# Optimization experiments

Measured on AMD Instinct MI355X. Metric: run time of the kernel, lower is better.

Reference implementation:

```python
import jax, jax.numpy as jnp
import numpy as np

B, SEG, MEM, D, E, H = 4, 1024, 1024, 128, 128, 8  # model_dim == embed_dim required by module
TOTAL = SEG + MEM


def sinusoid_pos(length, e):
    # Transformer-XL relative sinusoid table, then flipped so row 0 = largest distance
    p = jnp.arange(length, dtype=jnp.float32)[:, None]
    j = jnp.arange(e, dtype=jnp.float32)[None, :]
    ang = p / jnp.power(jnp.float32(10000.0), 2.0 * j / e)
    enc = jnp.where((jnp.arange(e) % 2 == 0)[None, :], jnp.sin(ang), jnp.cos(ang))
    return enc[::-1]


def circulant_shift(b, shift):
    # b: (B, H, S, W). Row i of the index matrix is the rolled arange shifted by (shift - i).
    W = b.shape[-1]
    S = b.shape[-2]
    idx = jnp.roll(jnp.arange(W), shift)[::-1]
    idx2 = jnp.concatenate([idx, idx])
    win = idx2[jnp.arange(S)[:, None] + jnp.arange(W)[None, :]][:, ::-1]  # (S, W)
    return jnp.take_along_axis(b, win[None, None, :, :], axis=3)


def setup_inputs() -> dict:
    key = jax.random.key(0)
    ks = jax.random.split(key, 11)
    w = 0.02  # small init for linear weights (Linear default-ish scale)
    return {
        "x": jax.random.normal(ks[0], (B, SEG, D), dtype=jnp.float32),
        "mem": jax.random.normal(ks[1], (B, MEM, D), dtype=jnp.float32),
        "att_mask": jnp.zeros((SEG, TOTAL), dtype=bool),  # unused by the module's forward
        "u1": jax.random.normal(ks[2], (H, 1, E), dtype=jnp.float32),
        "u2": jax.random.normal(ks[3], (H, 1, E), dtype=jnp.float32),
        "w_q": jax.random.normal(ks[4], (D, H * E), dtype=jnp.float32) * w,
        "w_kv": jax.random.normal(ks[5], (D, 2 * H * E), dtype=jnp.float32) * w,
        "w_r": jax.random.normal(ks[6], (D, H * E), dtype=jnp.float32) * w,
        "w_mlp": jax.random.normal(ks[7], (H * E, D), dtype=jnp.float32) * w,
        "ln_g": jnp.ones((D,), dtype=jnp.float32),
        "ln_b": jnp.zeros((D,), dtype=jnp.float32),
    }


def reference(x, mem, att_mask, u1, u2, w_q, w_kv, w_r, w_mlp, ln_g, ln_b):
    bsz, seg, d = x.shape
    h = jnp.concatenate((mem, x), axis=1)          # (B, total, D)
    total = h.shape[1]
    mem_len = total - seg

    # NB: the original uses .view without transpose -> plain row-major reshape
    q = (x @ w_q).reshape(bsz, -1, seg, d)          # (B, H, S, E)
    kv = (h @ w_kv).reshape(2 * bsz, -1, total, d)  # (2B, H, T, E)
    k, v = kv[:bsz], kv[bsz:]

    pos = sinusoid_pos(total, d)                    # buffer pos[-total:]
    r = (pos @ w_r).reshape(-1, total, d)           # (H, T, E)

    b = jnp.einsum('bhse,hte->bhst', q, r)
    b = circulant_shift(b, -seg + 1)

    qk = jnp.einsum('bhse,bhte->bhst', q, k)
    u1k = jnp.einsum('he,bhte->bht', u1[:, 0], k)[:, :, None, :]
    u2r = jnp.einsum('he,hte->ht', u2[:, 0], r)[None, :, None, :]

    score = qk + b + u1k + u2r                      # (B, H, S, T)
    tri = (jnp.arange(total)[None, :] - jnp.arange(seg)[:, None]) <= mem_len
    score = jnp.where(tri[None, None], score, 0.0) / jnp.sqrt(jnp.float32(d))
    score = jnp.where(score == 0.0, -jnp.inf, score)  # faithful zeros->-inf trick
    score = jax.nn.softmax(score, axis=-1)

    att = jnp.einsum('bhst,bhte->bhse', score, v).reshape(bsz, seg, -1)
    y = att @ w_mlp + x
    mu = jnp.mean(y, axis=-1, keepdims=True)
    var = jnp.mean((y - mu) ** 2, axis=-1, keepdims=True)
    return (y - mu) / jnp.sqrt(var + 1e-5) * ln_g + ln_b
```

## Files before the change

### kernel.cpp

```cpp
#include <hip/hip_runtime.h>
#include <hip/hip_bf16.h>
#include <stdint.h>

typedef __bf16 bf16;
typedef __attribute__((ext_vector_type(8))) __bf16 bf16x8;
typedef __attribute__((ext_vector_type(4))) float f32x4;

#define KSC 0.12764932952880681f

__device__ __forceinline__ f32x4 MFMA(bf16x8 a, bf16x8 b, f32x4 c) {
  return __builtin_amdgcn_mfma_f32_16x16x32_bf16(a, b, c, 0, 0, 0);
}

__device__ __forceinline__ void GLL16(const void* g, void* l) {
  __builtin_amdgcn_global_load_lds(
      (const __attribute__((address_space(1))) void*)g,
      (__attribute__((address_space(3))) void*)l, 16, 0, 0);
}

__device__ __forceinline__ bf16 tobf(float f) { return (bf16)f; }

__global__ __launch_bounds__(256) void k_prep(
    const float* __restrict__ x, const float* __restrict__ mm,
    const float* __restrict__ wq, const float* __restrict__ wkv,
    const float* __restrict__ wr, const float* __restrict__ wmlp,
    bf16* __restrict__ posb, bf16* __restrict__ wq_bt, bf16* __restrict__ wkv_bt,
    bf16* __restrict__ wr_bt, bf16* __restrict__ wmlp_bt,
    bf16* __restrict__ xb, bf16* __restrict__ memb)
{
  int id = blockIdx.x * 256 + threadIdx.x;
  if (id < 262144) {
    int t = id >> 7, j = id & 127;
    float p = (float)(2047 - t);
    float ang = p * exp2f(-(float)j * 0.20762050593046264f);
    float v = ((j & 1) == 0) ? sinf(ang) : cosf(ang);
    posb[id] = tobf(v);
    return;
  }
  id -= 262144;
  if (id < 131072) { int n = id >> 7, k = id & 127; wq_bt[id] = tobf(wq[k * 1024 + n]); return; }
  id -= 131072;
  if (id < 262144) { int n = id >> 7, k = id & 127; wkv_bt[id] = tobf(wkv[k * 2048 + n]); return; }
  id -= 262144;
  if (id < 131072) { int n = id >> 7, k = id & 127; wr_bt[id] = tobf(wr[k * 1024 + n]); return; }
  id -= 131072;
  if (id < 131072) { int n = id >> 10, k = id & 1023; wmlp_bt[id] = tobf(wmlp[k * 128 + n]); return; }
  id -= 131072;
  if (id < 524288) { xb[id] = tobf(x[id]); return; }
  id -= 524288;
  if (id < 524288) { memb[id] = tobf(mm[id]); return; }
}

template <int MODE>
__global__ __launch_bounds__(256, 2) void k_proj(
    const bf16* __restrict__ asrc, const bf16* __restrict__ asrc2,
    const bf16* __restrict__ wbt, bf16* __restrict__ out0, bf16* __restrict__ out1,
    float oscale)
{
  __shared__ bf16 As[64 * 128];
  __shared__ bf16 Bs[128 * 128];
  const int m0 = blockIdx.x * 64;
  const int n0 = blockIdx.y * 128;
  const int tid = threadIdx.x;
  const int w = tid >> 6, lane = tid & 63, g = lane >> 4, c = lane & 15;

#pragma unroll
  for (int it = 0; it < 4; ++it) {
    int ch = w * 256 + it * 64 + lane;
    int row = ch >> 4, cc = ch & 15;
    int scc = cc ^ (row & 7);
    const bf16* src;
    if (MODE == 1) {
      int rg = m0 + row;
      int bb = rg >> 11, t = rg & 2047;
      src = (t < 1024) ? (asrc2 + (size_t)(bb * 1024 + t) * 128)
                       : (asrc + (size_t)(bb * 1024 + (t - 1024)) * 128);
    } else {
      src = asrc + (size_t)(m0 + row) * 128;
    }
    GLL16(src + scc * 8, (char*)As + (w * 256 + it * 64) * 16);
  }
#pragma unroll
  for (int it = 0; it < 8; ++it) {
    int ch = w * 512 + it * 64 + lane;
    int n = ch >> 4, cc = ch & 15;
    int scc = cc ^ (n & 7);
    GLL16(wbt + (size_t)(n0 + n) * 128 + scc * 8, (char*)Bs + (w * 512 + it * 64) * 16);
  }
  __syncthreads();

  f32x4 acc[8] = {};
#pragma unroll
  for (int kk = 0; kk < 4; ++kk) {
    bf16x8 a = *(const bf16x8*)((const char*)As + (16 * w + c) * 256 + (((4 * kk + g) ^ (c & 7)) << 4));
#pragma unroll
    for (int fo = 0; fo < 8; ++fo) {
      bf16x8 b = *(const bf16x8*)((const char*)Bs + (16 * fo + c) * 256 + (((4 * kk + g) ^ (c & 7)) << 4));
      acc[fo] = MFMA(a, b, acc[fo]);
    }
  }

#pragma unroll
  for (int fo = 0; fo < 8; ++fo) {
#pragma unroll
    for (int j = 0; j < 4; ++j) {
      int rg = m0 + 16 * w + 4 * g + j;
      int cg = n0 + 16 * fo + c;
      bf16 v = tobf(acc[fo][j] * oscale);
      if (MODE == 0) {
        int b = rg >> 10, s2 = rg & 1023;
        int nn = s2 >> 7;
        int s = ((s2 & 127) << 3) | (cg >> 7);
        int e = cg & 127;
        out0[((size_t)((b * 8 + nn) * 1024 + s)) * 128 + e] = v;
      } else if (MODE == 1) {
        int bb = rg >> 11, t = rg & 2047;
        int nn = (t >> 7) & 7;
        int hlf = (t >> 10) & 1;
        int t2 = ((t & 127) << 4) | (cg >> 7);
        int e = cg & 127;
        if (bb < 2)
          out0[((size_t)(((2 * bb + hlf) * 8 + nn) * 2048 + t2)) * 128 + e] = v;
        else
          out1[((size_t)(((2 * (bb - 2) + hlf) * 8 + nn) * 2048 + t2)) * 128 + e] = v;
      } else {
        int nn = rg >> 8;
        int t = ((rg & 255) << 3) | (cg >> 7);
        int e = cg & 127;
        out0[((size_t)(nn * 2048 + t)) * 128 + e] = v;
      }
    }
  }
}

__global__ __launch_bounds__(256) void k_vtrans(const bf16* __restrict__ vh, bf16* __restrict__ vht)
{
  __shared__ bf16 T[64][72];
  int bt = blockIdx.x * 64, be = blockIdx.y * 64, bh = blockIdx.z;
  const bf16* src = vh + (size_t)bh * 2048 * 128;
  bf16* dst = vht + (size_t)bh * 128 * 2048;
#pragma unroll
  for (int i2 = 0; i2 < 2; ++i2) {
    int ch = i2 * 256 + threadIdx.x;
    int tt = ch >> 3, cc = ch & 7;
    bf16x8 v = *(const bf16x8*)(src + (size_t)(bt + tt) * 128 + be + cc * 8);
    *(bf16x8*)&T[tt][cc * 8] = v;
  }
  __syncthreads();
#pragma unroll
  for (int i2 = 0; i2 < 2; ++i2) {
    int ch = i2 * 256 + threadIdx.x;
    int ee = ch >> 3, c2 = ch & 7;
    bf16x8 o;
#pragma unroll
    for (int m = 0; m < 8; ++m) o[m] = T[c2 * 8 + m][ee];
    *(bf16x8*)(dst + (size_t)(be + ee) * 2048 + bt + c2 * 8) = o;
  }
}

__global__ __launch_bounds__(256) void k_uterms(
    const bf16* __restrict__ kh, const bf16* __restrict__ rh,
    const float* __restrict__ u1, const float* __restrict__ u2,
    float* __restrict__ uu)
{
  int id = blockIdx.x * 256 + threadIdx.x;
  int n = (id >> 11) & 7;
  int t = id & 2047;
  const bf16* kp = kh + (size_t)id * 128;
  const bf16* rp = rh + ((size_t)(n * 2048 + t)) * 128;
  const float* u1p = u1 + n * 128;
  const float* u2p = u2 + n * 128;
  float s = 0.f;
#pragma unroll
  for (int c0 = 0; c0 < 128; c0 += 8) {
    bf16x8 kv = *(const bf16x8*)(kp + c0);
    bf16x8 rv = *(const bf16x8*)(rp + c0);
#pragma unroll
    for (int j = 0; j < 8; ++j) s += (float)kv[j] * u1p[c0 + j] + (float)rv[j] * u2p[c0 + j];
  }
  uu[id] = s * KSC;
}

__global__ __launch_bounds__(256, 2) void k_flash(
    const bf16* __restrict__ qh, const bf16* __restrict__ kh,
    const bf16* __restrict__ vht, const bf16* __restrict__ rh,
    const float* __restrict__ uu, bf16* __restrict__ att2)
{
  __shared__ bf16 Ks[2][64 * 128];
  __shared__ bf16 Vs[2][64 * 128];
  __shared__ bf16 QRS[4][16 * 90];

  const int x = blockIdx.x;
  const int bh = x & 31;
  const int qb = (x < 256) ? (x >> 5) : (15 - ((x - 256) >> 5));
  const int ib = bh >> 3, nh = bh & 7;
  const int s0 = qb * 64;
  const int tid = threadIdx.x;
  const int w = tid >> 6, lane = tid & 63, g = lane >> 4, c = lane & 15;

  const bf16* qbase = qh + (size_t)bh * 1024 * 128;
  const bf16* kbase = kh + (size_t)bh * 2048 * 128;
  const bf16* vbase = vht + (size_t)bh * 128 * 2048;
  const bf16* rbase = rh + (size_t)nh * 2048 * 128;
  const float* uup  = uu + bh * 2048;

  const int nt = qb + 17;

  auto stage = [&](int tile) {
    int pb = tile & 1;
    int t0s = tile * 64;
    char* Kd = (char*)Ks[pb];
    char* Vd = (char*)Vs[pb];
#pragma unroll
    for (int it = 0; it < 4; ++it) {
      int ch = w * 256 + it * 64 + lane;
      int row = ch >> 4, cc2 = ch & 15;
      GLL16(kbase + (size_t)(t0s + row) * 128 + ((cc2 ^ (row & 7)) * 8), Kd + ch * 16);
    }
#pragma unroll
    for (int it = 0; it < 4; ++it) {
      int ch = w * 256 + it * 64 + lane;
      int e = ch >> 3, tc = ch & 7;
      GLL16(vbase + (size_t)e * 2048 + t0s + ((tc ^ (e & 7)) * 8), Vd + ch * 16);
    }
  };

  bf16x8 qf[4];
  {
    int srow = s0 + 16 * w + c;
#pragma unroll
    for (int kk = 0; kk < 4; ++kk)
      qf[kk] = *(const bf16x8*)(qbase + (size_t)srow * 128 + kk * 32 + g * 8);
  }

  f32x4 Ot[8] = {};
  float m_j[4], l_j[4];
#pragma unroll
  for (int j = 0; j < 4; ++j) { m_j[j] = -1e30f; l_j[j] = 0.f; }

  stage(0);

  for (int tt = 0; tt < nt; ++tt) {
    const int t0 = tt * 64;
    const int pb = tt & 1;
    __syncthreads();
    if (tt + 1 < nt) stage(tt + 1);

    bf16x8 rf[5][4];
    const int wb = t0 - s0 - 16 * w - 1040 + 4096;
#pragma unroll
    for (int f2 = 0; f2 < 5; ++f2) {
      int u = (wb + 16 * f2 + c) & 2047;
      const bf16* rrow = rbase + (size_t)u * 128;
#pragma unroll
      for (int kk = 0; kk < 4; ++kk) rf[f2][kk] = *(const bf16x8*)(rrow + kk * 32 + g * 8);
    }

    const bf16* Kc = Ks[pb];
    const bf16* Vc = Vs[pb];

    f32x4 sacc[4] = {};
    __builtin_amdgcn_s_setprio(1);
#pragma unroll
    for (int kk = 0; kk < 4; ++kk) {
#pragma unroll
      for (int f = 0; f < 4; ++f) {
        bf16x8 kf = *(const bf16x8*)((const char*)Kc + (16 * f + c) * 256 + (((4 * kk + g) ^ (c & 7)) << 4));
        sacc[f] = MFMA(qf[kk], kf, sacc[f]);
      }
    }
    f32x4 bacc[5] = {};
#pragma unroll
    for (int f2 = 0; f2 < 5; ++f2)
#pragma unroll
      for (int kk = 0; kk < 4; ++kk)
        bacc[f2] = MFMA(qf[kk], rf[f2][kk], bacc[f2]);
    __builtin_amdgcn_s_setprio(0);

    bf16* qrw = QRS[w];
#pragma unroll
    for (int f2 = 0; f2 < 5; ++f2)
#pragma unroll
      for (int j = 0; j < 4; ++j)
        qrw[(4 * g + j) * 90 + 16 * f2 + c] = tobf(bacc[f2][j]);

    float uuv[4];
#pragma unroll
    for (int f = 0; f < 4; ++f) uuv[f] = uup[t0 + 16 * f + c];

    const bool lastT = (tt == nt - 1);
    float zv[4][4];
#pragma unroll
    for (int f = 0; f < 4; ++f) {
#pragma unroll
      for (int j = 0; j < 4; ++j) {
        int il = 4 * g + j;
        float bias = (float)qrw[il * 90 + (16 * f + c - il + 15)];
        float z = sacc[f][j] + bias + uuv[f];
        if (lastT && (16 * f + c > 16 * w + il)) z = -1e30f;
        zv[f][j] = z;
      }
    }
    float alpha[4];
#pragma unroll
    for (int j = 0; j < 4; ++j) {
      float tm = fmaxf(fmaxf(zv[0][j], zv[1][j]), fmaxf(zv[2][j], zv[3][j]));
#pragma unroll
      for (int d = 1; d < 16; d <<= 1) tm = fmaxf(tm, __shfl_xor(tm, d));
      float mn = fmaxf(m_j[j], tm);
      alpha[j] = exp2f(m_j[j] - mn);
      m_j[j] = mn;
      float ps = 0.f;
#pragma unroll
      for (int f = 0; f < 4; ++f) { float pp = exp2f(zv[f][j] - mn); zv[f][j] = pp; ps += pp; }
#pragma unroll
      for (int d = 1; d < 16; d <<= 1) ps += __shfl_xor(ps, d);
      l_j[j] = l_j[j] * alpha[j] + ps;
    }
#pragma unroll
    for (int fo = 0; fo < 8; ++fo)
#pragma unroll
      for (int j = 0; j < 4; ++j) Ot[fo][j] *= alpha[j];

    bf16* pw = qrw;
#pragma unroll
    for (int f = 0; f < 4; ++f)
#pragma unroll
      for (int j = 0; j < 4; ++j) {
        int il = 4 * g + j;
        pw[il * 64 + ((((2 * f + (c >> 3)) ^ (il & 7)) << 3) | (c & 7))] = tobf(zv[f][j]);
      }

    __builtin_amdgcn_s_setprio(1);
#pragma unroll
    for (int kk2 = 0; kk2 < 2; ++kk2) {
      bf16x8 pa = *(const bf16x8*)(pw + c * 64 + (((4 * kk2 + g) ^ (c & 7)) << 3));
#pragma unroll
      for (int fo = 0; fo < 8; ++fo) {
        int e = 16 * fo + c;
        bf16x8 vf = *(const bf16x8*)((const char*)Vc + e * 128 + (((4 * kk2 + g) ^ (c & 7)) << 4));
        Ot[fo] = MFMA(pa, vf, Ot[fo]);
      }
    }
    __builtin_amdgcn_s_setprio(0);
  }

  bf16* ob = att2 + (size_t)ib * 1024 * 1024;
#pragma unroll
  for (int j = 0; j < 4; ++j) {
    int sg = s0 + 16 * w + 4 * g + j;
    size_t rowb = (size_t)(nh * 128 + (sg >> 3)) * 1024 + ((sg & 7) << 7);
    float inv = 1.f / l_j[j];
#pragma unroll
    for (int fo = 0; fo < 8; ++fo)
      ob[rowb + 16 * fo + c] = tobf(Ot[fo][j] * inv);
  }
}

__global__ __launch_bounds__(256, 2) void k_mlp(
    const bf16* __restrict__ att2, const bf16* __restrict__ wmlp_bt,
    const float* __restrict__ x, const float* __restrict__ lng, const float* __restrict__ lnb,
    float* __restrict__ out)
{
  __shared__ bf16 As[64 * 128];
  __shared__ bf16 Bs[128 * 128];
  const int m0 = blockIdx.x * 64;
  const int tid = threadIdx.x;
  const int w = tid >> 6, lane = tid & 63, g = lane >> 4, c = lane & 15;

  f32x4 acc[8] = {};
  for (int ks = 0; ks < 8; ++ks) {
    int k0 = ks * 128;
    __syncthreads();
#pragma unroll
    for (int it = 0; it < 4; ++it) {
      int ch = w * 256 + it * 64 + lane;
      int row = ch >> 4, cc = ch & 15;
      GLL16(att2 + (size_t)(m0 + row) * 1024 + k0 + ((cc ^ (row & 7)) * 8),
            (char*)As + (w * 256 + it * 64) * 16);
    }
#pragma unroll
    for (int it = 0; it < 8; ++it) {
      int ch = w * 512 + it * 64 + lane;
      int n = ch >> 4, cc = ch & 15;
      GLL16(wmlp_bt + (size_t)n * 1024 + k0 + ((cc ^ (n & 7)) * 8),
            (char*)Bs + (w * 512 + it * 64) * 16);
    }
    __syncthreads();
#pragma unroll
    for (int kk = 0; kk < 4; ++kk) {
      bf16x8 a = *(const bf16x8*)((const char*)As + (16 * w + c) * 256 + (((4 * kk + g) ^ (c & 7)) << 4));
#pragma unroll
      for (int fo = 0; fo < 8; ++fo) {
        bf16x8 b = *(const bf16x8*)((const char*)Bs + (16 * fo + c) * 256 + (((4 * kk + g) ^ (c & 7)) << 4));
        acc[fo] = MFMA(a, b, acc[fo]);
      }
    }
  }
#pragma unroll
  for (int j = 0; j < 4; ++j) {
    int rg = m0 + 16 * w + 4 * g + j;
    float y[8];
    float s1 = 0.f, s2 = 0.f;
#pragma unroll
    for (int fo = 0; fo < 8; ++fo) {
      float v = acc[fo][j] + x[(size_t)rg * 128 + 16 * fo + c];
      y[fo] = v; s1 += v; s2 += v * v;
    }
#pragma unroll
    for (int d = 1; d < 16; d <<= 1) { s1 += __shfl_xor(s1, d); s2 += __shfl_xor(s2, d); }
    float mu = s1 * 0.0078125f;
    float var = s2 * 0.0078125f - mu * mu;
    float rs = rsqrtf(var + 1e-5f);
#pragma unroll
    for (int fo = 0; fo < 8; ++fo) {
      int e = 16 * fo + c;
      out[(size_t)rg * 128 + e] = (y[fo] - mu) * rs * lng[e] + lnb[e];
    }
  }
}

extern "C" void kernel_launch(void* const* d_in, const int* in_sizes, int n_in,
                              void* d_out, int out_size, void* d_ws, size_t ws_size,
                              hipStream_t stream)
{
  const float* x    = (const float*)d_in[0];
  const float* mm   = (const float*)d_in[1];
  const float* u1   = (const float*)d_in[3];
  const float* u2   = (const float*)d_in[4];
  const float* wq   = (const float*)d_in[5];
  const float* wkv  = (const float*)d_in[6];
  const float* wr   = (const float*)d_in[7];
  const float* wmlp = (const float*)d_in[8];
  const float* lng  = (const float*)d_in[9];
  const float* lnb  = (const float*)d_in[10];
  float* out = (float*)d_out;

  char* p = (char*)d_ws;
  bf16* posb    = (bf16*)p;  p += (size_t)262144 * 2;
  bf16* wq_bt   = (bf16*)p;  p += (size_t)131072 * 2;
  bf16* wkv_bt  = (bf16*)p;  p += (size_t)262144 * 2;
  bf16* wr_bt   = (bf16*)p;  p += (size_t)131072 * 2;
  bf16* wmlp_bt = (bf16*)p;  p += (size_t)131072 * 2;
  bf16* xb      = (bf16*)p;  p += (size_t)524288 * 2;
  bf16* memb    = (bf16*)p;  p += (size_t)524288 * 2;
  bf16* qh      = (bf16*)p;  p += (size_t)4 * 8 * 1024 * 128 * 2;
  bf16* kh      = (bf16*)p;  p += (size_t)4 * 8 * 2048 * 128 * 2;
  bf16* vh      = (bf16*)p;  p += (size_t)4 * 8 * 2048 * 128 * 2;
  bf16* vht     = (bf16*)p;  p += (size_t)4 * 8 * 2048 * 128 * 2;
  bf16* rh      = (bf16*)p;  p += (size_t)8 * 2048 * 128 * 2;
  float* uu     = (float*)p; p += (size_t)65536 * 4;
  bf16* att2    = (bf16*)p;  p += (size_t)4 * 1024 * 1024 * 2;

  k_prep<<<dim3(7680), dim3(256), 0, stream>>>(x, mm, wq, wkv, wr, wmlp,
                                               posb, wq_bt, wkv_bt, wr_bt, wmlp_bt, xb, memb);
  k_proj<0><<<dim3(64, 8),   dim3(256), 0, stream>>>(xb,  (const bf16*)nullptr, wq_bt,  qh, (bf16*)nullptr, KSC);
  k_proj<1><<<dim3(128, 16), dim3(256), 0, stream>>>(xb,  memb,                 wkv_bt, kh, vh,             1.0f);
  k_proj<2><<<dim3(32, 8),   dim3(256), 0, stream>>>(posb,(const bf16*)nullptr, wr_bt,  rh, (bf16*)nullptr, 1.0f);
  k_vtrans<<<dim3(32, 2, 32), dim3(256), 0, stream>>>(vh, vht);
  k_uterms<<<dim3(256), dim3(256), 0, stream>>>(kh, rh, u1, u2, uu);
  k_flash<<<dim3(512), dim3(256), 0, stream>>>(qh, kh, vht, rh, uu, att2);
  k_mlp<<<dim3(64), dim3(256), 0, stream>>>(att2, wmlp_bt, x, lng, lnb, out);
}
```

Baseline: 318.4 us.

## Prefetch R tiles across iterations, merge aux kernels, vectorize prep conversions

In the flash kernel, the next iteration's relative-position R fragments and u-terms are now prefetched during the current iteration, and the last R fragment is reused from the previous window, so global loads stop sitting on the critical path. The softmax reductions are restructured so all four rows' shuffles are interleaved, which raises instruction-level parallelism. The V transpose and u-term kernels are fused into one launch. The prep kernel now reads weights coalesced and converts x/mem with vector loads. The prefetch raises register pressure in the flash kernel, which could reduce occupancy.

```diff
diff --git a/kernel.cpp b/kernel.cpp
--- a/kernel.cpp
+++ b/kernel.cpp
@@ -4,6 +4,7 @@
 
 typedef __bf16 bf16;
 typedef __attribute__((ext_vector_type(8))) __bf16 bf16x8;
+typedef __attribute__((ext_vector_type(4))) __bf16 bf16x4;
 typedef __attribute__((ext_vector_type(4))) float f32x4;
 
 #define KSC 0.12764932952880681f
@@ -38,17 +39,26 @@
     return;
   }
   id -= 262144;
-  if (id < 131072) { int n = id >> 7, k = id & 127; wq_bt[id] = tobf(wq[k * 1024 + n]); return; }
+  if (id < 131072) { int k = id >> 10, n = id & 1023; wq_bt[n * 128 + k] = tobf(wq[id]); return; }
   id -= 131072;
-  if (id < 262144) { int n = id >> 7, k = id & 127; wkv_bt[id] = tobf(wkv[k * 2048 + n]); return; }
+  if (id < 262144) { int k = id >> 11, n = id & 2047; wkv_bt[n * 128 + k] = tobf(wkv[id]); return; }
   id -= 262144;
-  if (id < 131072) { int n = id >> 7, k = id & 127; wr_bt[id] = tobf(wr[k * 1024 + n]); return; }
+  if (id < 131072) { int k = id >> 10, n = id & 1023; wr_bt[n * 128 + k] = tobf(wr[id]); return; }
   id -= 131072;
-  if (id < 131072) { int n = id >> 10, k = id & 1023; wmlp_bt[id] = tobf(wmlp[k * 128 + n]); return; }
+  if (id < 131072) { int k = id >> 7, n = id & 127; wmlp_bt[n * 1024 + k] = tobf(wmlp[id]); return; }
   id -= 131072;
-  if (id < 524288) { xb[id] = tobf(x[id]); return; }
-  id -= 524288;
-  if (id < 524288) { memb[id] = tobf(mm[id]); return; }
+  if (id < 131072) {
+    f32x4 v = *(const f32x4*)(x + (size_t)id * 4);
+    bf16x4 o; o[0]=tobf(v[0]); o[1]=tobf(v[1]); o[2]=tobf(v[2]); o[3]=tobf(v[3]);
+    *(bf16x4*)(xb + (size_t)id * 4) = o;
+    return;
+  }
+  id -= 131072;
+  if (id < 131072) {
+    f32x4 v = *(const f32x4*)(mm + (size_t)id * 4);
+    bf16x4 o; o[0]=tobf(v[0]); o[1]=tobf(v[1]); o[2]=tobf(v[2]); o[3]=tobf(v[3]);
+    *(bf16x4*)(memb + (size_t)id * 4) = o;
+  }
 }
 
 template <int MODE>
@@ -133,52 +143,53 @@
   }
 }
 
-__global__ __launch_bounds__(256) void k_vtrans(const bf16* __restrict__ vh, bf16* __restrict__ vht)
-{
-  __shared__ bf16 T[64][72];
-  int bt = blockIdx.x * 64, be = blockIdx.y * 64, bh = blockIdx.z;
-  const bf16* src = vh + (size_t)bh * 2048 * 128;
-  bf16* dst = vht + (size_t)bh * 128 * 2048;
-#pragma unroll
-  for (int i2 = 0; i2 < 2; ++i2) {
-    int ch = i2 * 256 + threadIdx.x;
-    int tt = ch >> 3, cc = ch & 7;
-    bf16x8 v = *(const bf16x8*)(src + (size_t)(bt + tt) * 128 + be + cc * 8);
-    *(bf16x8*)&T[tt][cc * 8] = v;
-  }
-  __syncthreads();
-#pragma unroll
-  for (int i2 = 0; i2 < 2; ++i2) {
-    int ch = i2 * 256 + threadIdx.x;
-    int ee = ch >> 3, c2 = ch & 7;
-    bf16x8 o;
-#pragma unroll
-    for (int m = 0; m < 8; ++m) o[m] = T[c2 * 8 + m][ee];
-    *(bf16x8*)(dst + (size_t)(be + ee) * 2048 + bt + c2 * 8) = o;
-  }
-}
-
-__global__ __launch_bounds__(256) void k_uterms(
+__global__ __launch_bounds__(256) void k_aux(
+    const bf16* __restrict__ vh, bf16* __restrict__ vht,
     const bf16* __restrict__ kh, const bf16* __restrict__ rh,
     const float* __restrict__ u1, const float* __restrict__ u2,
     float* __restrict__ uu)
 {
-  int id = blockIdx.x * 256 + threadIdx.x;
-  int n = (id >> 11) & 7;
-  int t = id & 2047;
-  const bf16* kp = kh + (size_t)id * 128;
-  const bf16* rp = rh + ((size_t)(n * 2048 + t)) * 128;
-  const float* u1p = u1 + n * 128;
-  const float* u2p = u2 + n * 128;
-  float s = 0.f;
-#pragma unroll
-  for (int c0 = 0; c0 < 128; c0 += 8) {
-    bf16x8 kv = *(const bf16x8*)(kp + c0);
-    bf16x8 rv = *(const bf16x8*)(rp + c0);
-#pragma unroll
-    for (int j = 0; j < 8; ++j) s += (float)kv[j] * u1p[c0 + j] + (float)rv[j] * u2p[c0 + j];
-  }
-  uu[id] = s * KSC;
+  __shared__ bf16 T[64][72];
+  const int bid = blockIdx.x;
+  if (bid < 2048) {
+    int bt = (bid & 31) * 64, be = ((bid >> 5) & 1) * 64, bh = bid >> 6;
+    const bf16* src = vh + (size_t)bh * 2048 * 128;
+    bf16* dst = vht + (size_t)bh * 128 * 2048;
+#pragma unroll
+    for (int i2 = 0; i2 < 2; ++i2) {
+      int ch = i2 * 256 + threadIdx.x;
+      int tt = ch >> 3, cc = ch & 7;
+      bf16x8 v = *(const bf16x8*)(src + (size_t)(bt + tt) * 128 + be + cc * 8);
+      *(bf16x8*)&T[tt][cc * 8] = v;
+    }
+    __syncthreads();
+#pragma unroll
+    for (int i2 = 0; i2 < 2; ++i2) {
+      int ch = i2 * 256 + threadIdx.x;
+      int ee = ch >> 3, c2 = ch & 7;
+      bf16x8 o;
+#pragma unroll
+      for (int m = 0; m < 8; ++m) o[m] = T[c2 * 8 + m][ee];
+      *(bf16x8*)(dst + (size_t)(be + ee) * 2048 + bt + c2 * 8) = o;
+    }
+  } else {
+    int id = (bid - 2048) * 256 + threadIdx.x;
+    int n = (id >> 11) & 7;
+    int t = id & 2047;
+    const bf16* kp = kh + (size_t)id * 128;
+    const bf16* rp = rh + ((size_t)(n * 2048 + t)) * 128;
+    const float* u1p = u1 + n * 128;
+    const float* u2p = u2 + n * 128;
+    float s = 0.f;
+#pragma unroll
+    for (int c0 = 0; c0 < 128; c0 += 8) {
+      bf16x8 kv = *(const bf16x8*)(kp + c0);
+      bf16x8 rv = *(const bf16x8*)(rp + c0);
+#pragma unroll
+      for (int j = 0; j < 8; ++j) s += (float)kv[j] * u1p[c0 + j] + (float)rv[j] * u2p[c0 + j];
+    }
+    uu[id] = s * KSC;
+  }
 }
 
 __global__ __launch_bounds__(256, 2) void k_flash(
@@ -233,6 +244,21 @@
       qf[kk] = *(const bf16x8*)(qbase + (size_t)srow * 128 + kk * 32 + g * 8);
   }
 
+  bf16x8 rf[5][4];
+  float uuv[4], uun[4];
+  {
+    const int wb0 = -s0 - 16 * w - 1040 + 4096;
+#pragma unroll
+    for (int f2 = 0; f2 < 5; ++f2) {
+      int u = (wb0 + 16 * f2 + c) & 2047;
+      const bf16* rrow = rbase + (size_t)u * 128;
+#pragma unroll
+      for (int kk = 0; kk < 4; ++kk) rf[f2][kk] = *(const bf16x8*)(rrow + kk * 32 + g * 8);
+    }
+#pragma unroll
+    for (int f = 0; f < 4; ++f) uuv[f] = uup[16 * f + c];
+  }
+
   f32x4 Ot[8] = {};
   float m_j[4], l_j[4];
 #pragma unroll
@@ -241,20 +267,10 @@
   stage(0);
 
   for (int tt = 0; tt < nt; ++tt) {
-    const int t0 = tt * 64;
     const int pb = tt & 1;
+    const bool notlast = (tt + 1 < nt);
     __syncthreads();
-    if (tt + 1 < nt) stage(tt + 1);
-
-    bf16x8 rf[5][4];
-    const int wb = t0 - s0 - 16 * w - 1040 + 4096;
-#pragma unroll
-    for (int f2 = 0; f2 < 5; ++f2) {
-      int u = (wb + 16 * f2 + c) & 2047;
-      const bf16* rrow = rbase + (size_t)u * 128;
-#pragma unroll
-      for (int kk = 0; kk < 4; ++kk) rf[f2][kk] = *(const bf16x8*)(rrow + kk * 32 + g * 8);
-    }
+    if (notlast) stage(tt + 1);
 
     const bf16* Kc = Ks[pb];
     const bf16* Vc = Vs[pb];
@@ -284,11 +300,22 @@
       for (int j = 0; j < 4; ++j)
         qrw[(4 * g + j) * 90 + 16 * f2 + c] = tobf(bacc[f2][j]);
 
-    float uuv[4];
-#pragma unroll
-    for (int f = 0; f < 4; ++f) uuv[f] = uup[t0 + 16 * f + c];
-
-    const bool lastT = (tt == nt - 1);
+    if (notlast) {
+#pragma unroll
+      for (int kk = 0; kk < 4; ++kk) rf[0][kk] = rf[4][kk];
+      const int wbn = 64 * (tt + 1) - s0 - 16 * w - 1040 + 4096;
+#pragma unroll
+      for (int f2 = 1; f2 < 5; ++f2) {
+        int u = (wbn + 16 * f2 + c) & 2047;
+        const bf16* rrow = rbase + (size_t)u * 128;
+#pragma unroll
+        for (int kk = 0; kk < 4; ++kk) rf[f2][kk] = *(const bf16x8*)(rrow + kk * 32 + g * 8);
+      }
+#pragma unroll
+      for (int f = 0; f < 4; ++f) uun[f] = uup[64 * (tt + 1) + 16 * f + c];
+    }
+
+    const bool lastT = !notlast;
     float zv[4][4];
 #pragma unroll
     for (int f = 0; f < 4; ++f) {
@@ -301,22 +328,32 @@
         zv[f][j] = z;
       }
     }
-    float alpha[4];
+    float tm[4], ps[4], alpha[4];
+#pragma unroll
+    for (int j = 0; j < 4; ++j)
+      tm[j] = fmaxf(fmaxf(zv[0][j], zv[1][j]), fmaxf(zv[2][j], zv[3][j]));
+#pragma unroll
+    for (int d = 1; d < 16; d <<= 1)
+#pragma unroll
+      for (int j = 0; j < 4; ++j) tm[j] = fmaxf(tm[j], __shfl_xor(tm[j], d));
 #pragma unroll
     for (int j = 0; j < 4; ++j) {
-      float tm = fmaxf(fmaxf(zv[0][j], zv[1][j]), fmaxf(zv[2][j], zv[3][j]));
-#pragma unroll
-      for (int d = 1; d < 16; d <<= 1) tm = fmaxf(tm, __shfl_xor(tm, d));
-      float mn = fmaxf(m_j[j], tm);
+      float mn = fmaxf(m_j[j], tm[j]);
       alpha[j] = exp2f(m_j[j] - mn);
       m_j[j] = mn;
-      float ps = 0.f;
-#pragma unroll
-      for (int f = 0; f < 4; ++f) { float pp = exp2f(zv[f][j] - mn); zv[f][j] = pp; ps += pp; }
-#pragma unroll
-      for (int d = 1; d < 16; d <<= 1) ps += __shfl_xor(ps, d);
-      l_j[j] = l_j[j] * alpha[j] + ps;
-    }
+    }
+#pragma unroll
+    for (int j = 0; j < 4; ++j) {
+      ps[j] = 0.f;
+#pragma unroll
+      for (int f = 0; f < 4; ++f) { float pp = exp2f(zv[f][j] - m_j[j]); zv[f][j] = pp; ps[j] += pp; }
+    }
+#pragma unroll
+    for (int d = 1; d < 16; d <<= 1)
+#pragma unroll
+      for (int j = 0; j < 4; ++j) ps[j] += __shfl_xor(ps[j], d);
+#pragma unroll
+    for (int j = 0; j < 4; ++j) l_j[j] = l_j[j] * alpha[j] + ps[j];
 #pragma unroll
     for (int fo = 0; fo < 8; ++fo)
 #pragma unroll
@@ -343,6 +380,9 @@
       }
     }
     __builtin_amdgcn_s_setprio(0);
+
+#pragma unroll
+    for (int f = 0; f < 4; ++f) uuv[f] = uun[f];
   }
 
   bf16* ob = att2 + (size_t)ib * 1024 * 1024;
@@ -452,13 +492,12 @@
   float* uu     = (float*)p; p += (size_t)65536 * 4;
   bf16* att2    = (bf16*)p;  p += (size_t)4 * 1024 * 1024 * 2;
 
-  k_prep<<<dim3(7680), dim3(256), 0, stream>>>(x, mm, wq, wkv, wr, wmlp,
+  k_prep<<<dim3(4608), dim3(256), 0, stream>>>(x, mm, wq, wkv, wr, wmlp,
                                                posb, wq_bt, wkv_bt, wr_bt, wmlp_bt, xb, memb);
   k_proj<0><<<dim3(64, 8),   dim3(256), 0, stream>>>(xb,  (const bf16*)nullptr, wq_bt,  qh, (bf16*)nullptr, KSC);
   k_proj<1><<<dim3(128, 16), dim3(256), 0, stream>>>(xb,  memb,                 wkv_bt, kh, vh,             1.0f);
   k_proj<2><<<dim3(32, 8),   dim3(256), 0, stream>>>(posb,(const bf16*)nullptr, wr_bt,  rh, (bf16*)nullptr, 1.0f);
-  k_vtrans<<<dim3(32, 2, 32), dim3(256), 0, stream>>>(vh, vht);
-  k_uterms<<<dim3(256), dim3(256), 0, stream>>>(kh, rh, u1, u2, uu);
+  k_aux<<<dim3(2304), dim3(256), 0, stream>>>(vh, vht, kh, rh, u1, u2, uu);
   k_flash<<<dim3(512), dim3(256), 0, stream>>>(qh, kh, vht, rh, uu, att2);
   k_mlp<<<dim3(64), dim3(256), 0, stream>>>(att2, wmlp_bt, x, lng, lnb, out);
 }
```

Result: faster. 308.8 us (-3.0%).

## Fold u-bias terms into shifted queries, drop uterms kernel, rework flash softmax

Applied to the files above, without the earlier changes.

The u1/u2 bias terms are folded algebraically into two pre-scaled query copies (q+u1 for the K product, q+u2 for the R product), which removes the separate k_uterms kernel and the per-tile uu loads. The R table is padded with 64 wrapped rows so the flash kernel can walk it with precomputed pointers and prefetch the next tile's R fragments, replacing the per-tile modulo addressing. MFMA operands are swapped so each lane owns one query row, the softmax uses a single running max with a lazy rescale that is skipped while the max grows by less than a threshold, and K/V staging uses precomputed incremental pointers. The prep kernel now uses coalesced reads for the weight transposes and vectorised x/mem conversion. These changes add a second query buffer and raise register pressure from prefetched R fragments.

```diff
diff --git a/kernel.cpp b/kernel.cpp
--- a/kernel.cpp
+++ b/kernel.cpp
@@ -4,6 +4,7 @@
 
 typedef __bf16 bf16;
 typedef __attribute__((ext_vector_type(8))) __bf16 bf16x8;
+typedef __attribute__((ext_vector_type(4))) __bf16 bf16x4;
 typedef __attribute__((ext_vector_type(4))) float f32x4;
 
 #define KSC 0.12764932952880681f
@@ -38,24 +39,33 @@
     return;
   }
   id -= 262144;
-  if (id < 131072) { int n = id >> 7, k = id & 127; wq_bt[id] = tobf(wq[k * 1024 + n]); return; }
+  if (id < 131072) { int k = id >> 10, n = id & 1023; wq_bt[n * 128 + k] = tobf(wq[id]); return; }
   id -= 131072;
-  if (id < 262144) { int n = id >> 7, k = id & 127; wkv_bt[id] = tobf(wkv[k * 2048 + n]); return; }
+  if (id < 262144) { int k = id >> 11, n = id & 2047; wkv_bt[n * 128 + k] = tobf(wkv[id]); return; }
   id -= 262144;
-  if (id < 131072) { int n = id >> 7, k = id & 127; wr_bt[id] = tobf(wr[k * 1024 + n]); return; }
+  if (id < 131072) { int k = id >> 10, n = id & 1023; wr_bt[n * 128 + k] = tobf(wr[id]); return; }
   id -= 131072;
-  if (id < 131072) { int n = id >> 10, k = id & 1023; wmlp_bt[id] = tobf(wmlp[k * 128 + n]); return; }
+  if (id < 131072) { int k = id >> 7, n = id & 127; wmlp_bt[n * 1024 + k] = tobf(wmlp[id]); return; }
   id -= 131072;
-  if (id < 524288) { xb[id] = tobf(x[id]); return; }
-  id -= 524288;
-  if (id < 524288) { memb[id] = tobf(mm[id]); return; }
+  if (id < 131072) {
+    f32x4 v = *(const f32x4*)(x + (size_t)id * 4);
+    bf16x4 o; o[0]=tobf(v[0]); o[1]=tobf(v[1]); o[2]=tobf(v[2]); o[3]=tobf(v[3]);
+    *(bf16x4*)(xb + (size_t)id * 4) = o;
+    return;
+  }
+  id -= 131072;
+  if (id < 131072) {
+    f32x4 v = *(const f32x4*)(mm + (size_t)id * 4);
+    bf16x4 o; o[0]=tobf(v[0]); o[1]=tobf(v[1]); o[2]=tobf(v[2]); o[3]=tobf(v[3]);
+    *(bf16x4*)(memb + (size_t)id * 4) = o;
+  }
 }
 
 template <int MODE>
 __global__ __launch_bounds__(256, 2) void k_proj(
     const bf16* __restrict__ asrc, const bf16* __restrict__ asrc2,
     const bf16* __restrict__ wbt, bf16* __restrict__ out0, bf16* __restrict__ out1,
-    float oscale)
+    const float* __restrict__ u1, const float* __restrict__ u2)
 {
   __shared__ bf16 As[64 * 128];
   __shared__ bf16 Bs[128 * 128];
@@ -106,19 +116,22 @@
     for (int j = 0; j < 4; ++j) {
       int rg = m0 + 16 * w + 4 * g + j;
       int cg = n0 + 16 * fo + c;
-      bf16 v = tobf(acc[fo][j] * oscale);
+      float av = acc[fo][j];
       if (MODE == 0) {
         int b = rg >> 10, s2 = rg & 1023;
         int nn = s2 >> 7;
         int s = ((s2 & 127) << 3) | (cg >> 7);
         int e = cg & 127;
-        out0[((size_t)((b * 8 + nn) * 1024 + s)) * 128 + e] = v;
+        size_t idx = ((size_t)((b * 8 + nn) * 1024 + s)) * 128 + e;
+        out0[idx] = tobf((av + u1[nn * 128 + e]) * KSC);
+        out1[idx] = tobf((av + u2[nn * 128 + e]) * KSC);
       } else if (MODE == 1) {
         int bb = rg >> 11, t = rg & 2047;
         int nn = (t >> 7) & 7;
         int hlf = (t >> 10) & 1;
         int t2 = ((t & 127) << 4) | (cg >> 7);
         int e = cg & 127;
+        bf16 v = tobf(av);
         if (bb < 2)
           out0[((size_t)(((2 * bb + hlf) * 8 + nn) * 2048 + t2)) * 128 + e] = v;
         else
@@ -127,7 +140,9 @@
         int nn = rg >> 8;
         int t = ((rg & 255) << 3) | (cg >> 7);
         int e = cg & 127;
-        out0[((size_t)(nn * 2048 + t)) * 128 + e] = v;
+        bf16 v = tobf(av);
+        out0[((size_t)(nn * 2112 + t)) * 128 + e] = v;
+        if (t < 64) out0[((size_t)(nn * 2112 + 2048 + t)) * 128 + e] = v;
       }
     }
   }
@@ -158,37 +173,14 @@
   }
 }
 
-__global__ __launch_bounds__(256) void k_uterms(
-    const bf16* __restrict__ kh, const bf16* __restrict__ rh,
-    const float* __restrict__ u1, const float* __restrict__ u2,
-    float* __restrict__ uu)
-{
-  int id = blockIdx.x * 256 + threadIdx.x;
-  int n = (id >> 11) & 7;
-  int t = id & 2047;
-  const bf16* kp = kh + (size_t)id * 128;
-  const bf16* rp = rh + ((size_t)(n * 2048 + t)) * 128;
-  const float* u1p = u1 + n * 128;
-  const float* u2p = u2 + n * 128;
-  float s = 0.f;
-#pragma unroll
-  for (int c0 = 0; c0 < 128; c0 += 8) {
-    bf16x8 kv = *(const bf16x8*)(kp + c0);
-    bf16x8 rv = *(const bf16x8*)(rp + c0);
-#pragma unroll
-    for (int j = 0; j < 8; ++j) s += (float)kv[j] * u1p[c0 + j] + (float)rv[j] * u2p[c0 + j];
-  }
-  uu[id] = s * KSC;
-}
-
 __global__ __launch_bounds__(256, 2) void k_flash(
-    const bf16* __restrict__ qh, const bf16* __restrict__ kh,
-    const bf16* __restrict__ vht, const bf16* __restrict__ rh,
-    const float* __restrict__ uu, bf16* __restrict__ att2)
+    const bf16* __restrict__ qhk, const bf16* __restrict__ qhr,
+    const bf16* __restrict__ kh, const bf16* __restrict__ vht,
+    const bf16* __restrict__ rhe, bf16* __restrict__ att2)
 {
   __shared__ bf16 Ks[2][64 * 128];
   __shared__ bf16 Vs[2][64 * 128];
-  __shared__ bf16 QRS[4][16 * 90];
+  __shared__ char QRS[4][2688];
 
   const int x = blockIdx.x;
   const int bh = x & 31;
@@ -198,66 +190,80 @@
   const int tid = threadIdx.x;
   const int w = tid >> 6, lane = tid & 63, g = lane >> 4, c = lane & 15;
 
-  const bf16* qbase = qh + (size_t)bh * 1024 * 128;
+  const bf16* qkb  = qhk + (size_t)bh * 1024 * 128;
+  const bf16* qrb  = qhr + (size_t)bh * 1024 * 128;
   const bf16* kbase = kh + (size_t)bh * 2048 * 128;
   const bf16* vbase = vht + (size_t)bh * 128 * 2048;
-  const bf16* rbase = rh + (size_t)nh * 2048 * 128;
-  const float* uup  = uu + bh * 2048;
+  const bf16* rbase = rhe + (size_t)nh * 2112 * 128;
 
   const int nt = qb + 17;
 
-  auto stage = [&](int tile) {
-    int pb = tile & 1;
-    int t0s = tile * 64;
-    char* Kd = (char*)Ks[pb];
-    char* Vd = (char*)Vs[pb];
-#pragma unroll
-    for (int it = 0; it < 4; ++it) {
-      int ch = w * 256 + it * 64 + lane;
-      int row = ch >> 4, cc2 = ch & 15;
-      GLL16(kbase + (size_t)(t0s + row) * 128 + ((cc2 ^ (row & 7)) * 8), Kd + ch * 16);
-    }
-#pragma unroll
-    for (int it = 0; it < 4; ++it) {
-      int ch = w * 256 + it * 64 + lane;
-      int e = ch >> 3, tc = ch & 7;
-      GLL16(vbase + (size_t)e * 2048 + t0s + ((tc ^ (e & 7)) * 8), Vd + ch * 16);
-    }
+  const bf16 *kp0, *kp1, *vp0, *vp1, *vp2, *vp3;
+  {
+    int ch0 = w * 256 + lane;
+    int ch1 = ch0 + 64;
+    int r0 = ch0 >> 4, cc0 = ch0 & 15;
+    int r1 = ch1 >> 4, cc1 = ch1 & 15;
+    kp0 = kbase + (size_t)r0 * 128 + (cc0 ^ (r0 & 7)) * 8;
+    kp1 = kbase + (size_t)r1 * 128 + (cc1 ^ (r1 & 7)) * 8;
+    int e0 = ch0 >> 3, t0c = ch0 & 7;
+    int e1 = ch1 >> 3, t1c = ch1 & 7;
+    int e2 = e0 + 16, e3 = e1 + 16;
+    vp0 = vbase + (size_t)e0 * 2048 + (t0c ^ (e0 & 7)) * 8;
+    vp1 = vbase + (size_t)e1 * 2048 + (t1c ^ (e1 & 7)) * 8;
+    vp2 = vbase + (size_t)e2 * 2048 + (t0c ^ (e2 & 7)) * 8;
+    vp3 = vbase + (size_t)e3 * 2048 + (t1c ^ (e3 & 7)) * 8;
+  }
+  const int dof = (w * 256 + lane) * 16;
+
+  auto stage = [&](char* Kd, char* Vd) {
+    GLL16(kp0, Kd + dof);
+    GLL16(kp1, Kd + dof + 1024);
+    GLL16(kp0 + 1024, Kd + dof + 2048);
+    GLL16(kp1 + 1024, Kd + dof + 3072);
+    GLL16(vp0, Vd + dof);
+    GLL16(vp1, Vd + dof + 1024);
+    GLL16(vp2, Vd + dof + 2048);
+    GLL16(vp3, Vd + dof + 3072);
+    kp0 += 8192; kp1 += 8192;
+    vp0 += 64; vp1 += 64; vp2 += 64; vp3 += 64;
   };
 
-  bf16x8 qf[4];
+  bf16x8 qfK[4], qfR[4];
   {
     int srow = s0 + 16 * w + c;
 #pragma unroll
-    for (int kk = 0; kk < 4; ++kk)
-      qf[kk] = *(const bf16x8*)(qbase + (size_t)srow * 128 + kk * 32 + g * 8);
+    for (int kk = 0; kk < 4; ++kk) {
+      qfK[kk] = *(const bf16x8*)(qkb + (size_t)srow * 128 + kk * 32 + g * 8);
+      qfR[kk] = *(const bf16x8*)(qrb + (size_t)srow * 128 + kk * 32 + g * 8);
+    }
+  }
+
+  bf16x8 rf[5][4];
+  const bf16* rp[5];
+  {
+    const int L0 = 1008 - s0 - 16 * w + c;
+#pragma unroll
+    for (int f2 = 0; f2 < 5; ++f2) {
+      rp[f2] = rbase + (size_t)(L0 + 16 * f2) * 128 + g * 8;
+#pragma unroll
+      for (int kk = 0; kk < 4; ++kk) rf[f2][kk] = *(const bf16x8*)(rp[f2] + kk * 32);
+      rp[f2] += 64 * 128;
+    }
   }
 
   f32x4 Ot[8] = {};
-  float m_j[4], l_j[4];
-#pragma unroll
-  for (int j = 0; j < 4; ++j) { m_j[j] = -1e30f; l_j[j] = 0.f; }
-
-  stage(0);
+  float m_r = -1e30f, l_r = 0.f;
+
+  stage((char*)Ks[0], (char*)Vs[0]);
 
   for (int tt = 0; tt < nt; ++tt) {
-    const int t0 = tt * 64;
-    const int pb = tt & 1;
     __syncthreads();
-    if (tt + 1 < nt) stage(tt + 1);
-
-    bf16x8 rf[5][4];
-    const int wb = t0 - s0 - 16 * w - 1040 + 4096;
-#pragma unroll
-    for (int f2 = 0; f2 < 5; ++f2) {
-      int u = (wb + 16 * f2 + c) & 2047;
-      const bf16* rrow = rbase + (size_t)u * 128;
-#pragma unroll
-      for (int kk = 0; kk < 4; ++kk) rf[f2][kk] = *(const bf16x8*)(rrow + kk * 32 + g * 8);
-    }
-
-    const bf16* Kc = Ks[pb];
-    const bf16* Vc = Vs[pb];
+    const bool notlast = (tt + 1 < nt);
+    if (notlast) stage((char*)Ks[(tt + 1) & 1], (char*)Vs[(tt + 1) & 1]);
+
+    const bf16* Kc = Ks[tt & 1];
+    const bf16* Vc = Vs[tt & 1];
 
     f32x4 sacc[4] = {};
     __builtin_amdgcn_s_setprio(1);
@@ -266,7 +272,7 @@
 #pragma unroll
       for (int f = 0; f < 4; ++f) {
         bf16x8 kf = *(const bf16x8*)((const char*)Kc + (16 * f + c) * 256 + (((4 * kk + g) ^ (c & 7)) << 4));
-        sacc[f] = MFMA(qf[kk], kf, sacc[f]);
+        sacc[f] = MFMA(kf, qfK[kk], sacc[f]);
       }
     }
     f32x4 bacc[5] = {};
@@ -274,67 +280,80 @@
     for (int f2 = 0; f2 < 5; ++f2)
 #pragma unroll
       for (int kk = 0; kk < 4; ++kk)
-        bacc[f2] = MFMA(qf[kk], rf[f2][kk], bacc[f2]);
+        bacc[f2] = MFMA(rf[f2][kk], qfR[kk], bacc[f2]);
     __builtin_amdgcn_s_setprio(0);
 
-    bf16* qrw = QRS[w];
+    bf16* qrw = (bf16*)QRS[w];
 #pragma unroll
     for (int f2 = 0; f2 < 5; ++f2)
 #pragma unroll
       for (int j = 0; j < 4; ++j)
-        qrw[(4 * g + j) * 90 + 16 * f2 + c] = tobf(bacc[f2][j]);
-
-    float uuv[4];
-#pragma unroll
-    for (int f = 0; f < 4; ++f) uuv[f] = uup[t0 + 16 * f + c];
-
-    const bool lastT = (tt == nt - 1);
+        qrw[c * 82 + 16 * f2 + 4 * g + j] = tobf(bacc[f2][j]);
+
+    if (notlast) {
+#pragma unroll
+      for (int f2 = 0; f2 < 5; ++f2) {
+#pragma unroll
+        for (int kk = 0; kk < 4; ++kk) rf[f2][kk] = *(const bf16x8*)(rp[f2] + kk * 32);
+        rp[f2] += 64 * 128;
+      }
+    }
+
     float zv[4][4];
 #pragma unroll
-    for (int f = 0; f < 4; ++f) {
+    for (int f = 0; f < 4; ++f)
 #pragma unroll
       for (int j = 0; j < 4; ++j) {
-        int il = 4 * g + j;
-        float bias = (float)qrw[il * 90 + (16 * f + c - il + 15)];
-        float z = sacc[f][j] + bias + uuv[f];
-        if (lastT && (16 * f + c > 16 * w + il)) z = -1e30f;
+        int tl = 16 * f + 4 * g + j;
+        float z = sacc[f][j] + (float)qrw[c * 82 + (tl - c + 15)];
+        if (!notlast && (tl > 16 * w + c)) z = -1e30f;
         zv[f][j] = z;
       }
-    }
-    float alpha[4];
-#pragma unroll
-    for (int j = 0; j < 4; ++j) {
-      float tm = fmaxf(fmaxf(zv[0][j], zv[1][j]), fmaxf(zv[2][j], zv[3][j]));
-#pragma unroll
-      for (int d = 1; d < 16; d <<= 1) tm = fmaxf(tm, __shfl_xor(tm, d));
-      float mn = fmaxf(m_j[j], tm);
-      alpha[j] = exp2f(m_j[j] - mn);
-      m_j[j] = mn;
-      float ps = 0.f;
-#pragma unroll
-      for (int f = 0; f < 4; ++f) { float pp = exp2f(zv[f][j] - mn); zv[f][j] = pp; ps += pp; }
-#pragma unroll
-      for (int d = 1; d < 16; d <<= 1) ps += __shfl_xor(ps, d);
-      l_j[j] = l_j[j] * alpha[j] + ps;
-    }
-#pragma unroll
-    for (int fo = 0; fo < 8; ++fo)
-#pragma unroll
-      for (int j = 0; j < 4; ++j) Ot[fo][j] *= alpha[j];
-
-    bf16* pw = qrw;
+
+    float pm = fmaxf(fmaxf(fmaxf(zv[0][0], zv[0][1]), fmaxf(zv[0][2], zv[0][3])),
+                     fmaxf(fmaxf(zv[1][0], zv[1][1]), fmaxf(zv[1][2], zv[1][3])));
+    float pm2 = fmaxf(fmaxf(fmaxf(zv[2][0], zv[2][1]), fmaxf(zv[2][2], zv[2][3])),
+                      fmaxf(fmaxf(zv[3][0], zv[3][1]), fmaxf(zv[3][2], zv[3][3])));
+    pm = fmaxf(pm, pm2);
+    pm = fmaxf(pm, __shfl_xor(pm, 16));
+    pm = fmaxf(pm, __shfl_xor(pm, 32));
+
+    float alpha = 1.f;
+    if (!__all(pm <= m_r + 8.0f)) {
+      float mn = fmaxf(m_r, pm);
+      alpha = exp2f(m_r - mn);
+      m_r = mn;
+      float at[4];
+#pragma unroll
+      for (int j = 0; j < 4; ++j) at[j] = __shfl(alpha, 20 * g + j);
+#pragma unroll
+      for (int fo = 0; fo < 8; ++fo)
+#pragma unroll
+        for (int j = 0; j < 4; ++j) Ot[fo][j] *= at[j];
+    }
+
+    float ps = 0.f;
 #pragma unroll
     for (int f = 0; f < 4; ++f)
 #pragma unroll
+      for (int j = 0; j < 4; ++j) { float pp = exp2f(zv[f][j] - m_r); zv[f][j] = pp; ps += pp; }
+    ps += __shfl_xor(ps, 16);
+    ps += __shfl_xor(ps, 32);
+    l_r = l_r * alpha + ps;
+
+    bf16* pw = (bf16*)QRS[w];
+#pragma unroll
+    for (int f = 0; f < 4; ++f)
+#pragma unroll
       for (int j = 0; j < 4; ++j) {
-        int il = 4 * g + j;
-        pw[il * 64 + ((((2 * f + (c >> 3)) ^ (il & 7)) << 3) | (c & 7))] = tobf(zv[f][j]);
+        int t = 16 * f + 4 * g + j;
+        pw[c * 80 + ((((t >> 3) ^ (c & 7)) << 3) | (t & 7))] = tobf(zv[f][j]);
       }
 
     __builtin_amdgcn_s_setprio(1);
 #pragma unroll
     for (int kk2 = 0; kk2 < 2; ++kk2) {
-      bf16x8 pa = *(const bf16x8*)(pw + c * 64 + (((4 * kk2 + g) ^ (c & 7)) << 3));
+      bf16x8 pa = *(const bf16x8*)(pw + c * 80 + (((4 * kk2 + g) ^ (c & 7)) << 3));
 #pragma unroll
       for (int fo = 0; fo < 8; ++fo) {
         int e = 16 * fo + c;
@@ -345,15 +364,17 @@
     __builtin_amdgcn_s_setprio(0);
   }
 
+  float linv[4];
+#pragma unroll
+  for (int j = 0; j < 4; ++j) linv[j] = 1.f / __shfl(l_r, 20 * g + j);
   bf16* ob = att2 + (size_t)ib * 1024 * 1024;
 #pragma unroll
   for (int j = 0; j < 4; ++j) {
     int sg = s0 + 16 * w + 4 * g + j;
     size_t rowb = (size_t)(nh * 128 + (sg >> 3)) * 1024 + ((sg & 7) << 7);
-    float inv = 1.f / l_j[j];
 #pragma unroll
     for (int fo = 0; fo < 8; ++fo)
-      ob[rowb + 16 * fo + c] = tobf(Ot[fo][j] * inv);
+      ob[rowb + 16 * fo + c] = tobf(Ot[fo][j] * linv[j]);
   }
 }
 
@@ -444,21 +465,20 @@
   bf16* wmlp_bt = (bf16*)p;  p += (size_t)131072 * 2;
   bf16* xb      = (bf16*)p;  p += (size_t)524288 * 2;
   bf16* memb    = (bf16*)p;  p += (size_t)524288 * 2;
-  bf16* qh      = (bf16*)p;  p += (size_t)4 * 8 * 1024 * 128 * 2;
+  bf16* qhk     = (bf16*)p;  p += (size_t)4 * 8 * 1024 * 128 * 2;
+  bf16* qhr     = (bf16*)p;  p += (size_t)4 * 8 * 1024 * 128 * 2;
   bf16* kh      = (bf16*)p;  p += (size_t)4 * 8 * 2048 * 128 * 2;
   bf16* vh      = (bf16*)p;  p += (size_t)4 * 8 * 2048 * 128 * 2;
   bf16* vht     = (bf16*)p;  p += (size_t)4 * 8 * 2048 * 128 * 2;
-  bf16* rh      = (bf16*)p;  p += (size_t)8 * 2048 * 128 * 2;
-  float* uu     = (float*)p; p += (size_t)65536 * 4;
+  bf16* rhe     = (bf16*)p;  p += (size_t)8 * 2112 * 128 * 2;
   bf16* att2    = (bf16*)p;  p += (size_t)4 * 1024 * 1024 * 2;
 
-  k_prep<<<dim3(7680), dim3(256), 0, stream>>>(x, mm, wq, wkv, wr, wmlp,
+  k_prep<<<dim3(4608), dim3(256), 0, stream>>>(x, mm, wq, wkv, wr, wmlp,
                                                posb, wq_bt, wkv_bt, wr_bt, wmlp_bt, xb, memb);
-  k_proj<0><<<dim3(64, 8),   dim3(256), 0, stream>>>(xb,  (const bf16*)nullptr, wq_bt,  qh, (bf16*)nullptr, KSC);
-  k_proj<1><<<dim3(128, 16), dim3(256), 0, stream>>>(xb,  memb,                 wkv_bt, kh, vh,             1.0f);
-  k_proj<2><<<dim3(32, 8),   dim3(256), 0, stream>>>(posb,(const bf16*)nullptr, wr_bt,  rh, (bf16*)nullptr, 1.0f);
+  k_proj<0><<<dim3(64, 8),   dim3(256), 0, stream>>>(xb,  (const bf16*)nullptr, wq_bt,  qhk, qhr, u1, u2);
+  k_proj<1><<<dim3(128, 16), dim3(256), 0, stream>>>(xb,  memb,                 wkv_bt, kh,  vh,  nullptr, nullptr);
+  k_proj<2><<<dim3(32, 8),   dim3(256), 0, stream>>>(posb,(const bf16*)nullptr, wr_bt,  rhe, (bf16*)nullptr, nullptr, nullptr);
   k_vtrans<<<dim3(32, 2, 32), dim3(256), 0, stream>>>(vh, vht);
-  k_uterms<<<dim3(256), dim3(256), 0, stream>>>(kh, rh, u1, u2, uu);
-  k_flash<<<dim3(512), dim3(256), 0, stream>>>(qh, kh, vht, rh, uu, att2);
+  k_flash<<<dim3(512), dim3(256), 0, stream>>>(qhk, qhr, kh, vht, rhe, att2);
   k_mlp<<<dim3(64), dim3(256), 0, stream>>>(att2, wmlp_bt, x, lng, lnb, out);
 }
```

Measured after the change: 273.9 us. 14.0% less time.
